# Kernel tuning notes

Hardware: AMD Instinct MI355X
Metric: run time of the kernel (lower is better)

## Reference

```python
import jax, jax.numpy as jnp
import numpy as np

IN_FEATURES = 4096
OUT_FEATURES = 4096
GROUP_SIZE = 128
N_GROUPS = IN_FEATURES // GROUP_SIZE
N_LEVELS = 16
SCALE = float(np.sqrt(GROUP_SIZE))


def setup_inputs() -> dict:
    key = jax.random.key(0)
    k_x, k_idx, k_cb, k_norm, k_rot = jax.random.split(key, 5)
    x = jax.random.normal(k_x, (4, 2048, IN_FEATURES), dtype=jnp.float32)
    # packed 4-bit indices: each uint8 byte holds two 4-bit codes (stored as int32 here)
    indices_packed = jax.random.randint(k_idx, (OUT_FEATURES, IN_FEATURES // 2), 0, 256, dtype=jnp.int32)
    codebook = jax.random.normal(k_cb, (N_LEVELS,), dtype=jnp.float32)
    weight_norms = jax.random.uniform(k_norm, (OUT_FEATURES, N_GROUPS), dtype=jnp.float32) + 0.5
    # per-group random orthogonal rotations (QR of gaussian), matching generate_rotation_matrix semantics
    g = jax.random.normal(k_rot, (N_GROUPS, GROUP_SIZE, GROUP_SIZE), dtype=jnp.float32)
    q, _ = jnp.linalg.qr(g)
    rotations = q.astype(jnp.float32)
    return {"x": x, "indices_packed": indices_packed, "codebook": codebook,
            "weight_norms": weight_norms, "rotations": rotations}


def _unpack_4bit(packed):
    # packed: (N, K//2) -> (N, K); even columns from low nibble, odd from high nibble
    low = packed & 0xF
    high = (packed >> 4) & 0xF
    return jnp.stack([low, high], axis=-1).reshape(packed.shape[0], -1)


def reference(x, indices_packed, codebook, weight_norms, rotations):
    B, S, K = x.shape
    xf = x.reshape(-1, K).astype(jnp.float32)            # (T, K)
    T = xf.shape[0]
    # group-wise rotation: x_rot_g = x_g @ Pi_g.T
    xg = xf.reshape(T, N_GROUPS, GROUP_SIZE)             # (T, G, g)
    x_rot = jnp.einsum('tgk,gjk->tgj', xg, rotations)    # (T, G, g)
    # dequantized codes (before norm scaling)
    idx = _unpack_4bit(indices_packed)                    # (N, K)
    W = codebook[idx].reshape(OUT_FEATURES, N_GROUPS, GROUP_SIZE)  # (N, G, g)
    # out[t,n] = sum_g (x_rot[t,g,:] . W[n,g,:]) * norms[n,g] / scale
    out = jnp.einsum('tgj,ngj,ng->tn', x_rot, W, weight_norms / SCALE)
    return out.reshape(B, S, OUT_FEATURES).astype(x.dtype)
```

## Files before the change

kernel.cpp:

```cpp
#include <hip/hip_runtime.h>

typedef __attribute__((ext_vector_type(8))) __bf16 bf16x8;
typedef __attribute__((ext_vector_type(4))) float f32x4;
typedef __attribute__((ext_vector_type(4))) int i32x4;
typedef __attribute__((ext_vector_type(8))) unsigned short ushort8;

#define T_TOKENS 8192
#define K_DIM    4096
#define N_DIM    4096
#define NGRP     32
#define GS       128

__device__ __forceinline__ unsigned short f2bf(float f) {
  unsigned u = __builtin_bit_cast(unsigned, f);
  u += 0x7fffu + ((u >> 16) & 1u);
  return (unsigned short)(u >> 16);
}

__device__ __forceinline__ f32x4 mfma16(bf16x8 a, bf16x8 b, f32x4 c) {
  return __builtin_amdgcn_mfma_f32_16x16x32_bf16(a, b, c, 0, 0, 0);
}

__device__ __forceinline__ i32x4 mfma_i8(i32x4 a, i32x4 b, i32x4 c) {
  return __builtin_amdgcn_mfma_i32_16x16x64_i8(a, b, c, 0, 0, 0);
}

__device__ __forceinline__ void gload_lds16(const void* g, void* l) {
  __builtin_amdgcn_global_load_lds(
      (const __attribute__((address_space(1))) void*)g,
      (__attribute__((address_space(3))) void*)l, 16, 0, 0);
}

__device__ __forceinline__ int clamp127(int q) {
  return q > 127 ? 127 : (q < -127 ? -127 : q);
}

__global__ __launch_bounds__(256) void k_prep(const float* __restrict__ x,
                                              signed char* __restrict__ qx,
                                              float* __restrict__ sxf,
                                              const int* __restrict__ idxp,
                                              const float* __restrict__ cb,
                                              const float* __restrict__ norms,
                                              const float* __restrict__ rot,
                                              unsigned short* __restrict__ weff,
                                              int* __restrict__ swmax) {
  __shared__ unsigned short Rt[128][136];
  __shared__ unsigned short Wq[128][136];
  __shared__ float cbl[16];
  const int tid = threadIdx.x;

  if (blockIdx.x < 2048) {
    const int wid = blockIdx.x * 4 + (tid >> 6);
    const int l = tid & 63;
    const float* xr = x + (size_t)wid * K_DIM;
    float4 v[16];
    float am = 0.f;
    #pragma unroll
    for (int i = 0; i < 16; ++i) {
      v[i] = *reinterpret_cast<const float4*>(xr + (i * 64 + l) * 4);
      am = fmaxf(am, fmaxf(fmaxf(fabsf(v[i].x), fabsf(v[i].y)),
                           fmaxf(fabsf(v[i].z), fabsf(v[i].w))));
    }
    #pragma unroll
    for (int m = 1; m < 64; m <<= 1) am = fmaxf(am, __shfl_xor(am, m, 64));
    const float inv = am > 0.f ? 127.0f / am : 0.f;
    #pragma unroll
    for (int i = 0; i < 16; ++i) {
      int q0 = clamp127(__float2int_rn(v[i].x * inv));
      int q1 = clamp127(__float2int_rn(v[i].y * inv));
      int q2 = clamp127(__float2int_rn(v[i].z * inv));
      int q3 = clamp127(__float2int_rn(v[i].w * inv));
      unsigned d = (q0 & 255) | ((q1 & 255) << 8) | ((q2 & 255) << 16) |
                   ((unsigned)(q3 & 255) << 24);
      *reinterpret_cast<unsigned*>(qx + (size_t)wid * K_DIM + (size_t)(i * 64 + l) * 4) = d;
    }
    if (l == 0) sxf[wid] = am * (1.0f / 127.0f);
    return;
  }

  const int v = blockIdx.x - 2048;
  const int nt = v & 31;
  const int g  = v >> 5;
  if (tid < 16) cbl[tid] = cb[tid];

  {
    const int j = tid >> 1, kh = (tid & 1) * 64;
    const float* rp = rot + ((size_t)g * 128 + j) * 128 + kh;
    #pragma unroll
    for (int c = 0; c < 64; c += 4) {
      float4 vv = *reinterpret_cast<const float4*>(rp + c);
      Rt[kh + c + 0][j] = f2bf(vv.x);
      Rt[kh + c + 1][j] = f2bf(vv.y);
      Rt[kh + c + 2][j] = f2bf(vv.z);
      Rt[kh + c + 3][j] = f2bf(vv.w);
    }
  }
  __syncthreads();

  {
    const int nl = tid >> 1, hf = (tid & 1);
    const int* ip = idxp + ((size_t)(nt * 128 + nl)) * (K_DIM / 2) + g * 64 + hf * 32;
    #pragma unroll
    for (int c = 0; c < 32; c += 4) {
      int4 vv = *reinterpret_cast<const int4*>(ip + c);
      int va[4] = {vv.x, vv.y, vv.z, vv.w};
      #pragma unroll
      for (int q = 0; q < 4; ++q) {
        int b = va[q] & 0xFF;
        Wq[nl][hf * 64 + (c + q) * 2 + 0] = f2bf(cbl[b & 0xF]);
        Wq[nl][hf * 64 + (c + q) * 2 + 1] = f2bf(cbl[(b >> 4) & 0xF]);
      }
    }
  }
  __syncthreads();

  const int w = tid >> 6, l = tid & 63;
  const int rl = l & 15, hi = l >> 4;
  f32x4 acc[2][8] = {};
  #pragma unroll
  for (int ks = 0; ks < 4; ++ks) {
    bf16x8 a0 = *(const bf16x8*)&Wq[w * 32 +  0 + rl][ks * 32 + hi * 8];
    bf16x8 a1 = *(const bf16x8*)&Wq[w * 32 + 16 + rl][ks * 32 + hi * 8];
    #pragma unroll
    for (int nc = 0; nc < 8; ++nc) {
      bf16x8 bfr = *(const bf16x8*)&Rt[nc * 16 + rl][ks * 32 + hi * 8];
      acc[0][nc] = mfma16(a0, bfr, acc[0][nc]);
      acc[1][nc] = mfma16(a1, bfr, acc[1][nc]);
    }
  }

  const float inv_scale = 0.088388347648318447f;
  #pragma unroll
  for (int m = 0; m < 2; ++m) {
    const int r0 = nt * 128 + w * 32 + m * 16 + hi * 4;
    float nv[4];
    #pragma unroll
    for (int r = 0; r < 4; ++r) nv[r] = norms[(size_t)(r0 + r) * NGRP + g] * inv_scale;
    float rowmax[4] = {0.f, 0.f, 0.f, 0.f};
    #pragma unroll
    for (int nc = 0; nc < 8; ++nc) {
      #pragma unroll
      for (int r = 0; r < 4; ++r) {
        float wv = acc[m][nc][r] * nv[r];
        weff[(size_t)(r0 + r) * K_DIM + g * GS + nc * 16 + rl] = f2bf(wv);
        rowmax[r] = fmaxf(rowmax[r], fabsf(wv));
      }
    }
    #pragma unroll
    for (int r = 0; r < 4; ++r) {
      #pragma unroll
      for (int msk = 1; msk < 16; msk <<= 1)
        rowmax[r] = fmaxf(rowmax[r], __shfl_xor(rowmax[r], msk, 64));
      if (rl == 0) atomicMax(&swmax[r0 + r], __float_as_int(rowmax[r]));
    }
  }
}

__global__ __launch_bounds__(256) void k_wquant(const unsigned short* __restrict__ weff,
                                                const int* __restrict__ swmax,
                                                signed char* __restrict__ qw,
                                                float* __restrict__ swf) {
  const int n = blockIdx.x, t = threadIdx.x;
  const float am = __int_as_float(swmax[n]);
  const float inv = am > 0.f ? 127.0f / am : 0.f;
  const unsigned short* wr = weff + (size_t)n * K_DIM + t * 16;
  ushort8 u0 = *(const ushort8*)wr;
  ushort8 u1 = *(const ushort8*)(wr + 8);
  unsigned d[4];
  #pragma unroll
  for (int j = 0; j < 2; ++j) {
    ushort8 u = j ? u1 : u0;
    #pragma unroll
    for (int h = 0; h < 2; ++h) {
      int q0 = clamp127(__float2int_rn(__uint_as_float((unsigned)u[h * 4 + 0] << 16) * inv));
      int q1 = clamp127(__float2int_rn(__uint_as_float((unsigned)u[h * 4 + 1] << 16) * inv));
      int q2 = clamp127(__float2int_rn(__uint_as_float((unsigned)u[h * 4 + 2] << 16) * inv));
      int q3 = clamp127(__float2int_rn(__uint_as_float((unsigned)u[h * 4 + 3] << 16) * inv));
      d[j * 2 + h] = (q0 & 255) | ((q1 & 255) << 8) | ((q2 & 255) << 16) |
                     ((unsigned)(q3 & 255) << 24);
    }
  }
  *reinterpret_cast<int4*>(qw + (size_t)n * K_DIM + t * 16) =
      make_int4((int)d[0], (int)d[1], (int)d[2], (int)d[3]);
  if (t == 0) swf[n] = am * (1.0f / 127.0f);
}

#define VMW asm volatile("s_waitcnt vmcnt(4)" ::: "memory")
#define NOW ((void)0)
#define BAR asm volatile("s_barrier" ::: "memory")

#define STG(gbase, koff, ldsoff) do { \
    gload_lds16((gbase) + (size_t)(koff), &lds[(ldsoff) + dst0]); \
    gload_lds16((gbase) + (size_t)(koff) + (size_t)64 * K_DIM, \
                &lds[(ldsoff) + dst0 + 4096]); \
  } while (0)

#define RD_B(PAR) { \
    const int bb = 32768 + (PAR) * 16384 + (wc >> 1) * 8192 + ((wc & 1) * 64 + rl) * 64; \
    _Pragma("unroll") \
    for (int n = 0; n < 4; ++n) { \
      bfr[n][0] = *(const i32x4*)&lds[bb + n * 1024 + slot0]; \
      bfr[n][1] = *(const i32x4*)&lds[bb + n * 1024 + slot1]; \
    } \
  }

#define RD_A(PAR, MQ, S) { \
    const int ab = (PAR) * 16384 + wr * 8192 + ((MQ) * 32 + rl) * 64; \
    S##0 = *(const i32x4*)&lds[ab + slot0]; \
    S##1 = *(const i32x4*)&lds[ab + slot1]; \
    S##2 = *(const i32x4*)&lds[ab + 1024 + slot0]; \
    S##3 = *(const i32x4*)&lds[ab + 1024 + slot1]; \
  }

#define MFMAQ(MQ, S) { \
    _Pragma("unroll") \
    for (int n = 0; n < 4; ++n) { \
      acc[(MQ)*2][n]     = mfma_i8(S##1, bfr[n][1], \
                             mfma_i8(S##0, bfr[n][0], acc[(MQ)*2][n])); \
      acc[(MQ)*2 + 1][n] = mfma_i8(S##3, bfr[n][1], \
                             mfma_i8(S##2, bfr[n][0], acc[(MQ)*2 + 1][n])); \
    } \
  }

#define PHASE2(qa, qb, PAR, RDB, TAIL, S1, S2) { \
    if (RDB) { RD_B(PAR) } \
    RD_A(PAR, qa, af) \
    RD_A(PAR, qb, ag) \
    S1; S2; \
    BAR; \
    __builtin_amdgcn_s_setprio(1); \
    MFMAQ(qa, af) \
    MFMAQ(qb, ag) \
    __builtin_amdgcn_s_setprio(0); \
    TAIL; \
    BAR; \
  }

__global__ __launch_bounds__(512) void k_gemm(const signed char* __restrict__ A,
                                              const signed char* __restrict__ Bw,
                                              const float* __restrict__ sxf,
                                              const float* __restrict__ swf,
                                              float* __restrict__ C) {
  __shared__ unsigned short lds[65536];
  const int tid = threadIdx.x;
  const int l = tid & 63, w = tid >> 6;
  const int wr = w >> 2, wc = w & 3;
  const int rl = l & 15, hi = l >> 4;

  const int bid = blockIdx.x;
  const int xcd = bid & 7, jj = bid >> 3;
  const int brow = ((xcd >> 1) * 8 + (jj >> 3)) * 256;
  const int bcol = ((xcd & 1) * 8 + (jj & 7)) * 256;

  const int row0 = tid >> 3;
  const int gc = ((tid & 7) ^ (row0 & 7)) * 16;
  const signed char* pa  = A  + (size_t)(brow + row0) * K_DIM + gc;
  const signed char* pa2 = pa + (size_t)128 * K_DIM;
  const signed char* pb  = Bw + (size_t)(bcol + row0) * K_DIM + gc;
  const signed char* pb2 = pb + (size_t)128 * K_DIM;
  const int dst0 = tid * 8;

  const int rb7 = rl & 7;
  const int slot0 = ((0 + hi) ^ rb7) << 3;
  const int slot1 = ((4 + hi) ^ rb7) << 3;

  i32x4 acc[8][4] = {};

  STG(pb,  0,   32768);
  STG(pb2, 0,   32768 + 8192);
  STG(pa,  0,   0);
  STG(pa2, 0,   8192);
  STG(pb,  128, 32768 + 16384);
  STG(pb2, 128, 32768 + 16384 + 8192);
  asm volatile("s_waitcnt vmcnt(4)" ::: "memory");
  asm volatile("s_barrier" ::: "memory");

  for (int it = 0; it < 16; ++it) {
    const int k0  = it * 256;
    const int kA1 = k0 + 128;
    const int kN0 = (k0 + 256) & (K_DIM - 1);
    const int kN1 = (k0 + 384) & (K_DIM - 1);
    i32x4 bfr[4][2];
    i32x4 af0, af1, af2, af3;
    i32x4 ag0, ag1, ag2, ag3;
    PHASE2(0, 1, 0, 1, NOW,
           STG(pa,  kA1, 16384),
           STG(pa2, kA1, 16384 + 8192))
    PHASE2(2, 3, 0, 0, VMW,
           STG(pb,  kN0, 32768),
           STG(pb2, kN0, 32768 + 8192))
    PHASE2(0, 1, 1, 1, NOW,
           STG(pa,  kN0, 0),
           STG(pa2, kN0, 8192))
    PHASE2(2, 3, 1, 0, VMW,
           STG(pb,  kN1, 32768 + 16384),
           STG(pb2, kN1, 32768 + 16384 + 8192))
  }

  float swv[4];
  #pragma unroll
  for (int n = 0; n < 4; ++n) swv[n] = swf[bcol + wc * 64 + n * 16 + rl];
  #pragma unroll
  for (int m = 0; m < 8; ++m) {
    const int row = brow + wr * 128 + m * 16 + hi * 4;
    float sxr[4];
    #pragma unroll
    for (int r = 0; r < 4; ++r) sxr[r] = sxf[row + r];
    #pragma unroll
    for (int n = 0; n < 4; ++n) {
      const int col = bcol + wc * 64 + n * 16 + rl;
      #pragma unroll
      for (int r = 0; r < 4; ++r)
        C[(size_t)(row + r) * N_DIM + col] = (float)acc[m][n][r] * sxr[r] * swv[n];
    }
  }
}

extern "C" void kernel_launch(void* const* d_in, const int* in_sizes, int n_in,
                              void* d_out, int out_size, void* d_ws, size_t ws_size,
                              hipStream_t stream) {
  const float* x     = (const float*)d_in[0];
  const int*   idxp  = (const int*)d_in[1];
  const float* cb    = (const float*)d_in[2];
  const float* norms = (const float*)d_in[3];
  const float* rot   = (const float*)d_in[4];
  float* out = (float*)d_out;

  unsigned short* weff = (unsigned short*)d_ws;
  signed char* qw  = (signed char*)d_ws + 33554432;
  signed char* qx  = (signed char*)d_ws + 50331648;
  float* sxf   = (float*)((char*)d_ws + 83886080);
  int*   swmax = (int*)((char*)d_ws + 83918848);
  float* swf   = (float*)((char*)d_ws + 83935232);

  hipMemsetAsync(swmax, 0, 16384, stream);
  k_prep<<<3072, 256, 0, stream>>>(x, qx, sxf, idxp, cb, norms, rot, weff, swmax);
  k_wquant<<<4096, 256, 0, stream>>>(weff, swmax, qw, swf);
  k_gemm<<<512, 512, 0, stream>>>(qx, qw, sxf, swf, out);
}
```

Baseline: 207.4 us.

## Restructure int8 GEMM main loop into 8 phases with A-fragment prefetch double-buffering

Splits each K-iteration into eight finer phases, each issuing one global-to-LDS stage and prefetching the next A fragment from LDS while MFMAs consume the previous one, ping-ponging between two register sets. The aim is to hide LDS read latency behind MFMA work and spread global loads more evenly. In exchange there are twice as many barriers per iteration. The moved wait/barrier placement also risks reading LDS data before it is ready.

```diff
diff --git a/kernel.cpp b/kernel.cpp
--- a/kernel.cpp
+++ b/kernel.cpp
@@ -222,17 +222,15 @@
     } \
   }
 
-#define PHASE2(qa, qb, PAR, RDB, TAIL, S1, S2) { \
-    if (RDB) { RD_B(PAR) } \
-    RD_A(PAR, qa, af) \
-    RD_A(PAR, qb, ag) \
-    S1; S2; \
+#define PHX(MQ, RDB_PAR, RDB, VM, STGS, RDN, S) { \
+    if (RDB) { RD_B(RDB_PAR) } \
+    STGS; \
+    VM; \
     BAR; \
+    RDN; \
     __builtin_amdgcn_s_setprio(1); \
-    MFMAQ(qa, af) \
-    MFMAQ(qb, ag) \
+    MFMAQ(MQ, S) \
     __builtin_amdgcn_s_setprio(0); \
-    TAIL; \
     BAR; \
   }
 
@@ -265,6 +263,9 @@
   const int slot1 = ((4 + hi) ^ rb7) << 3;
 
   i32x4 acc[8][4] = {};
+  i32x4 bfr[4][2];
+  i32x4 af0, af1, af2, af3;
+  i32x4 ag0, ag1, ag2, ag3;
 
   STG(pb,  0,   32768);
   STG(pb2, 0,   32768 + 8192);
@@ -274,27 +275,21 @@
   STG(pb2, 128, 32768 + 16384 + 8192);
   asm volatile("s_waitcnt vmcnt(4)" ::: "memory");
   asm volatile("s_barrier" ::: "memory");
+  RD_A(0, 0, af)
 
   for (int it = 0; it < 16; ++it) {
     const int k0  = it * 256;
     const int kA1 = k0 + 128;
     const int kN0 = (k0 + 256) & (K_DIM - 1);
     const int kN1 = (k0 + 384) & (K_DIM - 1);
-    i32x4 bfr[4][2];
-    i32x4 af0, af1, af2, af3;
-    i32x4 ag0, ag1, ag2, ag3;
-    PHASE2(0, 1, 0, 1, NOW,
-           STG(pa,  kA1, 16384),
-           STG(pa2, kA1, 16384 + 8192))
-    PHASE2(2, 3, 0, 0, VMW,
-           STG(pb,  kN0, 32768),
-           STG(pb2, kN0, 32768 + 8192))
-    PHASE2(0, 1, 1, 1, NOW,
-           STG(pa,  kN0, 0),
-           STG(pa2, kN0, 8192))
-    PHASE2(2, 3, 1, 0, VMW,
-           STG(pb,  kN1, 32768 + 16384),
-           STG(pb2, kN1, 32768 + 16384 + 8192))
+    PHX(0,   0,   1,  NOW, STG(pa,  kA1, 16384),              RD_A(0, 1, ag), af)
+    PHX(1,   0,   0,  NOW, STG(pa2, kA1, 16384 + 8192),       RD_A(0, 2, af), ag)
+    PHX(2,   0,   0,  NOW, STG(pb,  kN0, 32768),              RD_A(0, 3, ag), af)
+    PHX(3,   0,   0,  VMW, STG(pb2, kN0, 32768 + 8192),       RD_A(1, 0, af), ag)
+    PHX(0,   1,   1,  NOW, STG(pa,  kN0, 0),                  RD_A(1, 1, ag), af)
+    PHX(1,   1,   0,  NOW, STG(pa2, kN0, 8192),               RD_A(1, 2, af), ag)
+    PHX(2,   1,   0,  NOW, STG(pb,  kN1, 32768 + 16384),      RD_A(1, 3, ag), af)
+    PHX(3,   1,   0,  VMW, STG(pb2, kN1, 32768 + 16384 + 8192), RD_A(0, 0, af), ag)
   }
 
   float swv[4];
```

Result: no change. 207.4 us (+0.0%).
